# Performance work log

Hardware: AMD Instinct MI355X
Metric: run time of the kernel (lower is better)

## Reference

```python
import jax, jax.numpy as jnp
import numpy as np

L, NH, H, V, MAXP = 12, 12, 768, 50257, 1024
HD = H // NH
EPS = 1e-5


def setup_inputs() -> dict:
    key = jax.random.key(0)
    ks = iter(jax.random.split(key, 32))
    s = 0.02
    inp = {
        "input_ids": jax.random.randint(next(ks), (8, 1024), 0, V),
        "tok_emb": jax.random.normal(next(ks), (V, H), jnp.float32) * s,
        "pos_emb": jax.random.normal(next(ks), (MAXP, H), jnp.float32) * s,
        "ln1_g": jnp.ones((L, H), jnp.float32),
        "ln1_b": jnp.zeros((L, H), jnp.float32),
        "w_attn": jax.random.normal(next(ks), (L, H, 3 * H), jnp.float32) * s,
        "b_attn": jnp.zeros((L, 3 * H), jnp.float32),
        "w_out": jax.random.normal(next(ks), (L, H, H), jnp.float32) * s,
        "b_out": jnp.zeros((L, H), jnp.float32),
        "ln2_g": jnp.ones((L, H), jnp.float32),
        "ln2_b": jnp.zeros((L, H), jnp.float32),
        "w1": jax.random.normal(next(ks), (L, H, 4 * H), jnp.float32) * s,
        "b1": jnp.zeros((L, 4 * H), jnp.float32),
        "w2": jax.random.normal(next(ks), (L, 4 * H, H), jnp.float32) * s,
        "b2": jnp.zeros((L, H), jnp.float32),
        "lnf_g": jnp.ones((H,), jnp.float32),
        "lnf_b": jnp.zeros((H,), jnp.float32),
    }
    return inp


def _ln(x, g, b):
    mu = jnp.mean(x, axis=-1, keepdims=True)
    var = jnp.var(x, axis=-1, keepdims=True)
    return (x - mu) * jax.lax.rsqrt(var + EPS) * g + b


def _gpt2_forward(input_ids, tok_emb, pos_emb, ln1_g, ln1_b, w_attn, b_attn,
                  w_out, b_out, ln2_g, ln2_b, w1, b1, w2, b2, lnf_g, lnf_b):
    B, S = input_ids.shape
    x = tok_emb[input_ids] + pos_emb[:S]  # [B,S,H]
    # causal mask: True above the diagonal (future positions)
    mask = jnp.triu(jnp.ones((S, S), dtype=bool), k=1)
    inv_sqrt_hd = 1.0 / np.sqrt(HD)
    for l in range(L):
        n1 = _ln(x, ln1_g[l], ln1_b[l])
        qkv = n1 @ w_attn[l] + b_attn[l]  # [B,S,3H]
        q, k, v = jnp.split(qkv, 3, axis=-1)
        q = q.reshape(B, S, NH, HD).transpose(0, 2, 1, 3)
        k = k.reshape(B, S, NH, HD).transpose(0, 2, 1, 3)
        v = v.reshape(B, S, NH, HD).transpose(0, 2, 1, 3)
        scores = jnp.einsum('bhtd,bhsd->bhts', q, k)  # [B,NH,S,S]
        # faithful to source: mask with -10000 BEFORE dividing by sqrt(head_size)
        scores = jnp.where(mask, -10000.0, scores) * inv_sqrt_hd
        probs = jax.nn.softmax(scores, axis=-1)
        attn = jnp.einsum('bhts,bhsd->bhtd', probs, v)
        attn = attn.transpose(0, 2, 1, 3).reshape(B, S, H)
        attn = attn @ w_out[l] + b_out[l]
        x = x + attn
        n2 = _ln(x, ln2_g[l], ln2_b[l])
        h = jax.nn.gelu(n2 @ w1[l] + b1[l], approximate=False)
        x = x + (h @ w2[l] + b2[l])
    x = _ln(x, lnf_g, lnf_b)
    final_encoding = x[:, -1]  # [B,H]
    logits = final_encoding @ tok_emb.T  # tied weights, [B,V]
    return logits, final_encoding


def reference(input_ids, tok_emb, pos_emb, ln1_g, ln1_b, w_attn, b_attn,
              w_out, b_out, ln2_g, ln2_b, w1, b1, w2, b2, lnf_g, lnf_b):
    return _gpt2_forward(input_ids, tok_emb, pos_emb, ln1_g, ln1_b, w_attn,
                         b_attn, w_out, b_out, ln2_g, ln2_b, w1, b1, w2, b2,
                         lnf_g, lnf_b)
```

## Files before the change

kernel.cpp:

```cpp
#include <hip/hip_runtime.h>
#include <cmath>

typedef unsigned short u16;
typedef __bf16 bf16;
typedef __attribute__((ext_vector_type(8))) bf16 bf16x8;
typedef __attribute__((ext_vector_type(4))) float f32x4;

#define DINL __device__ __forceinline__

#define BB 8
#define SS 1024
#define HH 768
#define LL 12
#define NHH 12
#define HDD 64
#define MM 8192
#define VV 50257

DINL u16 f2bf(float f) {
    unsigned int u = __builtin_bit_cast(unsigned int, f);
    u += 0x7fff + ((u >> 16) & 1);
    return (u16)(u >> 16);
}

DINL bf16x8 ld_bf8(const u16* p) { return *(const bf16x8*)p; }

typedef __attribute__((address_space(1))) unsigned int as1_u32;
typedef __attribute__((address_space(3))) unsigned int as3_u32;

DINL void gllds16(const void* g, void* l) {
    __builtin_amdgcn_global_load_lds((as1_u32*)g, (as3_u32*)l, 16, 0, 0);
}

__global__ __launch_bounds__(256) void k_embed(const int* __restrict__ ids,
                                               const float* __restrict__ tok,
                                               const float* __restrict__ pos,
                                               float* __restrict__ x) {
    int tk = blockIdx.x;
    int s = tk & (SS - 1);
    int id = ids[tk];
    const float* tr = tok + (size_t)id * HH;
    const float* pr = pos + (size_t)s * HH;
    float* xr = x + (size_t)tk * HH;
#pragma unroll
    for (int j = 0; j < 3; j++) {
        int d = threadIdx.x + j * 256;
        xr[d] = tr[d] + pr[d];
    }
}

__global__ __launch_bounds__(256) void k_tcvt(const float* __restrict__ src, u16* __restrict__ dst,
                                              int R, int C, size_t sstr, size_t dstr) {
    src += (size_t)blockIdx.z * sstr;
    dst += (size_t)blockIdx.z * dstr;
    __shared__ float t[32][33];
    int tx = threadIdx.x & 31, ty = threadIdx.x >> 5;
    int c0 = blockIdx.x * 32, r0 = blockIdx.y * 32;
#pragma unroll
    for (int p = 0; p < 4; p++)
        t[ty + p * 8][tx] = src[(size_t)(r0 + ty + p * 8) * C + c0 + tx];
    __syncthreads();
#pragma unroll
    for (int p = 0; p < 4; p++)
        dst[(size_t)(c0 + ty + p * 8) * R + r0 + tx] = f2bf(t[tx][ty + p * 8]);
}

template <bool F32OUT>
__global__ __launch_bounds__(256) void k_ln(const float* __restrict__ x, const float* __restrict__ g,
                                            const float* __restrict__ b, void* __restrict__ outp,
                                            int nrows, int rs, int ro) {
    int w = threadIdx.x >> 6, lane = threadIdx.x & 63;
    int row = blockIdx.x * 4 + w;
    if (row >= nrows) return;
    const float4* xr = (const float4*)(x + ((size_t)row * rs + ro) * HH);
    float4 v[3];
    float s = 0.f, s2 = 0.f;
#pragma unroll
    for (int j = 0; j < 3; j++) {
        v[j] = xr[lane + 64 * j];
        s += v[j].x + v[j].y + v[j].z + v[j].w;
        s2 += v[j].x * v[j].x + v[j].y * v[j].y + v[j].z * v[j].z + v[j].w * v[j].w;
    }
#pragma unroll
    for (int off = 32; off; off >>= 1) {
        s += __shfl_xor(s, off, 64);
        s2 += __shfl_xor(s2, off, 64);
    }
    float mu = s * (1.0f / HH);
    float rstd = rsqrtf(s2 * (1.0f / HH) - mu * mu + 1e-5f);
#pragma unroll
    for (int j = 0; j < 3; j++) {
        int d4 = lane + 64 * j;
        float4 gv = ((const float4*)g)[d4];
        float4 bv = ((const float4*)b)[d4];
        float o0 = (v[j].x - mu) * rstd * gv.x + bv.x;
        float o1 = (v[j].y - mu) * rstd * gv.y + bv.y;
        float o2 = (v[j].z - mu) * rstd * gv.z + bv.z;
        float o3 = (v[j].w - mu) * rstd * gv.w + bv.w;
        if (F32OUT) {
            ((float4*)outp)[(size_t)row * (HH / 4) + d4] = make_float4(o0, o1, o2, o3);
        } else {
            ushort4 pk;
            pk.x = f2bf(o0); pk.y = f2bf(o1); pk.z = f2bf(o2); pk.w = f2bf(o3);
            *(ushort4*)((u16*)outp + (size_t)row * HH + d4 * 4) = pk;
        }
    }
}

template <int EPI>
__global__ __launch_bounds__(256) void k_gemm(const u16* __restrict__ A, const u16* __restrict__ BT,
                                              const float* __restrict__ bias, float* __restrict__ xio,
                                              u16* __restrict__ obuf, u16* __restrict__ qb,
                                              u16* __restrict__ kb, u16* __restrict__ vb,
                                              int N, int K) {
    __shared__ u16 As[2][128 * 32];
    __shared__ u16 Bs[2][128 * 32];
    const int t = threadIdx.x, w = t >> 6, lane = t & 63;
    const int l15 = lane & 15, l4 = lane >> 4;
    const int wr = w >> 1, wc = w & 1;
    const int m0 = blockIdx.y * 128, n0 = blockIdx.x * 128;
    const int KT = K >> 5;

    f32x4 acc[4][4] = {};

    auto stage = [&](int buf, int kt) {
#pragma unroll
        for (int i = 0; i < 2; i++) {
            int idx = w * 2 + i;
            int row = idx * 16 + (lane >> 2);
            int kc = kt * 32 + (((lane & 3) ^ ((lane >> 3) & 3)) * 8);
            gllds16(A + (size_t)(m0 + row) * K + kc, &As[buf][idx * 512]);
            gllds16(BT + (size_t)(n0 + row) * K + kc, &Bs[buf][idx * 512]);
        }
    };

    stage(0, 0);
    __syncthreads();
    int buf = 0;
    const int sw = (l15 >> 1) & 3;
    for (int kt = 0; kt < KT; ++kt) {
        if (kt + 1 < KT) stage(buf ^ 1, kt + 1);
        bf16x8 af[4], bfr[4];
#pragma unroll
        for (int i = 0; i < 4; i++) af[i] = ld_bf8(&As[buf][(wr * 64 + i * 16 + l15) * 32 + ((l4 ^ sw) * 8)]);
#pragma unroll
        for (int j = 0; j < 4; j++) bfr[j] = ld_bf8(&Bs[buf][(wc * 64 + j * 16 + l15) * 32 + ((l4 ^ sw) * 8)]);
#pragma unroll
        for (int i = 0; i < 4; i++)
#pragma unroll
            for (int j = 0; j < 4; j++)
                acc[i][j] = __builtin_amdgcn_mfma_f32_16x16x32_bf16(af[i], bfr[j], acc[i][j], 0, 0, 0);
        __syncthreads();
        buf ^= 1;
    }

#pragma unroll
    for (int i = 0; i < 4; i++) {
#pragma unroll
        for (int j = 0; j < 4; j++) {
#pragma unroll
            for (int r = 0; r < 4; r++) {
                int row = m0 + wr * 64 + i * 16 + l4 * 4 + r;
                int n = n0 + wc * 64 + j * 16 + l15;
                float v = acc[i][j][r] + bias[n];
                if (EPI == 0) {
                    int seg = n / HH, wi = n % HH;
                    int h = wi >> 6, d = wi & 63;
                    int bi = row >> 10, s = row & (SS - 1);
                    size_t bh = (size_t)(bi * NHH + h);
                    if (seg == 0)
                        qb[(bh * SS + s) * HDD + d] = f2bf(v);
                    else if (seg == 1)
                        kb[(bh * SS + s) * HDD + d] = f2bf(v);
                    else
                        vb[(bh * HDD + d) * SS + s] = f2bf(v);
                } else if (EPI == 1) {
                    xio[(size_t)row * N + n] += v;
                } else {
                    float gl = 0.5f * v * (1.0f + erff(v * 0.70710678118654752f));
                    obuf[(size_t)row * N + n] = f2bf(gl);
                }
            }
        }
    }
}

__global__ __launch_bounds__(256) void k_gemm64(const u16* __restrict__ A, const u16* __restrict__ BT,
                                                const float* __restrict__ bias, float* __restrict__ xio,
                                                int N, int K) {
    __shared__ u16 As[2][128 * 32];
    __shared__ u16 Bs[2][64 * 32];
    const int t = threadIdx.x, w = t >> 6, lane = t & 63;
    const int l15 = lane & 15, l4 = lane >> 4;
    const int wr = w >> 1, wc = w & 1;
    const int m0 = blockIdx.y * 128, n0 = blockIdx.x * 64;
    const int KT = K >> 5;

    f32x4 acc[4][2] = {};

    auto stage = [&](int buf, int kt) {
        int rr = lane >> 2;
        int kc = kt * 32 + (((lane & 3) ^ ((lane >> 3) & 3)) * 8);
#pragma unroll
        for (int i = 0; i < 2; i++) {
            int idx = w * 2 + i;
            gllds16(A + (size_t)(m0 + idx * 16 + rr) * K + kc, &As[buf][idx * 512]);
        }
        gllds16(BT + (size_t)(n0 + w * 16 + rr) * K + kc, &Bs[buf][w * 512]);
    };

    stage(0, 0);
    __syncthreads();
    int buf = 0;
    const int sw = (l15 >> 1) & 3;
    for (int kt = 0; kt < KT; ++kt) {
        if (kt + 1 < KT) stage(buf ^ 1, kt + 1);
        bf16x8 af[4], bfr[2];
#pragma unroll
        for (int i = 0; i < 4; i++) af[i] = ld_bf8(&As[buf][(wr * 64 + i * 16 + l15) * 32 + ((l4 ^ sw) * 8)]);
#pragma unroll
        for (int j = 0; j < 2; j++) bfr[j] = ld_bf8(&Bs[buf][(wc * 32 + j * 16 + l15) * 32 + ((l4 ^ sw) * 8)]);
#pragma unroll
        for (int i = 0; i < 4; i++)
#pragma unroll
            for (int j = 0; j < 2; j++)
                acc[i][j] = __builtin_amdgcn_mfma_f32_16x16x32_bf16(af[i], bfr[j], acc[i][j], 0, 0, 0);
        __syncthreads();
        buf ^= 1;
    }

#pragma unroll
    for (int i = 0; i < 4; i++) {
#pragma unroll
        for (int j = 0; j < 2; j++) {
#pragma unroll
            for (int r = 0; r < 4; r++) {
                int row = m0 + wr * 64 + i * 16 + l4 * 4 + r;
                int n = n0 + wc * 32 + j * 16 + l15;
                xio[(size_t)row * N + n] += acc[i][j][r] + bias[n];
            }
        }
    }
}

__global__ __launch_bounds__(256) void k_attn(const u16* __restrict__ q, const u16* __restrict__ k,
                                              const u16* __restrict__ vt, u16* __restrict__ o) {
    int qt = 15 - blockIdx.x;
    int bh = blockIdx.y;
    int w = threadIdx.x >> 6, lane = threadIdx.x & 63;
    int l15 = lane & 15, l4 = lane >> 4;

    __shared__ u16 Ks[2][64 * 64];
    __shared__ u16 Vs[2][64 * 64];
    __shared__ u16 pl[4][16 * 72];
    u16* pw = pl[w];

    const size_t bhq = (size_t)bh * SS * HDD;
    int qrow0 = qt * 64 + w * 16;

    auto stage = [&](int buf, int kvb) {
#pragma unroll
        for (int i = 0; i < 2; i++) {
            int rl = w * 16 + i * 8 + (lane >> 3);
            int c = lane & 7;
            int sc = (c ^ (rl & 7)) * 8;
            gllds16(k + bhq + (size_t)(kvb * 64 + rl) * HDD + sc, &Ks[buf][(w * 16 + i * 8) * 64]);
            gllds16(vt + ((size_t)bh * HDD + rl) * SS + kvb * 64 + sc, &Vs[buf][(w * 16 + i * 8) * 64]);
        }
    };

    bf16x8 aq[2];
#pragma unroll
    for (int ks = 0; ks < 2; ks++)
        aq[ks] = ld_bf8(q + bhq + (size_t)(qrow0 + l15) * HDD + ks * 32 + l4 * 8);

    f32x4 acc[4] = {};
    float mrun[4], lrun[4];
#pragma unroll
    for (int r = 0; r < 4; r++) { mrun[r] = -1e30f; lrun[r] = 0.f; }

    stage(0, 0);
    __syncthreads();
    int buf = 0;

    for (int kvb = 0; kvb <= qt; ++kvb) {
        if (kvb < qt) stage(buf ^ 1, kvb + 1);

        f32x4 s[4] = {};
#pragma unroll
        for (int c = 0; c < 4; c++) {
#pragma unroll
            for (int ks = 0; ks < 2; ks++) {
                bf16x8 kf = ld_bf8(&Ks[buf][(c * 16 + l15) * 64 + ((ks * 4 + l4) ^ (l15 & 7)) * 8]);
                s[c] = __builtin_amdgcn_mfma_f32_16x16x32_bf16(aq[ks], kf, s[c], 0, 0, 0);
            }
        }
        bool diag = (kvb == qt);
        float rmax[4] = {-1e30f, -1e30f, -1e30f, -1e30f};
#pragma unroll
        for (int c = 0; c < 4; c++) {
#pragma unroll
            for (int r = 0; r < 4; r++) {
                float val = s[c][r] * 0.125f;
                if (diag) {
                    int kvi = kvb * 64 + c * 16 + l15;
                    int qi = qrow0 + l4 * 4 + r;
                    if (kvi > qi) val = -1250.0f;
                }
                s[c][r] = val;
                rmax[r] = fmaxf(rmax[r], val);
            }
        }
#pragma unroll
        for (int off = 1; off < 16; off <<= 1)
#pragma unroll
            for (int r = 0; r < 4; r++) rmax[r] = fmaxf(rmax[r], __shfl_xor(rmax[r], off, 64));
        float ef[4];
#pragma unroll
        for (int r = 0; r < 4; r++) {
            float mnew = fmaxf(mrun[r], rmax[r]);
            ef[r] = __expf(mrun[r] - mnew);
            mrun[r] = mnew;
        }
        float rsum[4] = {0.f, 0.f, 0.f, 0.f};
#pragma unroll
        for (int c = 0; c < 4; c++)
#pragma unroll
            for (int r = 0; r < 4; r++) {
                float pv = __expf(s[c][r] - mrun[r]);
                s[c][r] = pv;
                rsum[r] += pv;
            }
#pragma unroll
        for (int off = 1; off < 16; off <<= 1)
#pragma unroll
            for (int r = 0; r < 4; r++) rsum[r] += __shfl_xor(rsum[r], off, 64);
#pragma unroll
        for (int r = 0; r < 4; r++) lrun[r] = lrun[r] * ef[r] + rsum[r];
#pragma unroll
        for (int cd = 0; cd < 4; cd++)
#pragma unroll
            for (int r = 0; r < 4; r++) acc[cd][r] *= ef[r];
#pragma unroll
        for (int c = 0; c < 4; c++)
#pragma unroll
            for (int r = 0; r < 4; r++)
                pw[(l4 * 4 + r) * 72 + c * 16 + l15] = f2bf(s[c][r]);
#pragma unroll
        for (int ks = 0; ks < 2; ks++) {
            bf16x8 pa = ld_bf8(pw + l15 * 72 + ks * 32 + l4 * 8);
#pragma unroll
            for (int cd = 0; cd < 4; cd++) {
                bf16x8 vf = ld_bf8(&Vs[buf][(cd * 16 + l15) * 64 + ((ks * 4 + l4) ^ (l15 & 7)) * 8]);
                acc[cd] = __builtin_amdgcn_mfma_f32_16x16x32_bf16(pa, vf, acc[cd], 0, 0, 0);
            }
        }
        __syncthreads();
        buf ^= 1;
    }

    int b = bh / NHH, h = bh % NHH;
#pragma unroll
    for (int cd = 0; cd < 4; cd++) {
#pragma unroll
        for (int r = 0; r < 4; r++) {
            int qi = qrow0 + l4 * 4 + r;
            float ov = acc[cd][r] / lrun[r];
            o[((size_t)b * SS + qi) * HH + h * HDD + cd * 16 + l15] = f2bf(ov);
        }
    }
}

__global__ __launch_bounds__(256) void k_logits(const float* __restrict__ enc,
                                                const float* __restrict__ tok,
                                                float* __restrict__ out) {
    int w = threadIdx.x >> 6, lane = threadIdx.x & 63;
    int v = blockIdx.x * 4 + w;
    if (v >= VV) return;
    const float4* tr = (const float4*)(tok + (size_t)v * HH);
    float a[8];
#pragma unroll
    for (int b = 0; b < 8; b++) a[b] = 0.f;
#pragma unroll
    for (int j = 0; j < 3; j++) {
        float4 t4 = tr[lane + 64 * j];
#pragma unroll
        for (int b = 0; b < 8; b++) {
            float4 e4 = *(const float4*)(enc + (size_t)b * HH + (lane + 64 * j) * 4);
            a[b] += t4.x * e4.x + t4.y * e4.y + t4.z * e4.z + t4.w * e4.w;
        }
    }
#pragma unroll
    for (int off = 32; off; off >>= 1)
#pragma unroll
        for (int b = 0; b < 8; b++) a[b] += __shfl_xor(a[b], off, 64);
    if (lane == 0) {
#pragma unroll
        for (int b = 0; b < 8; b++) out[(size_t)b * VV + v] = a[b];
    }
}

extern "C" void kernel_launch(void* const* d_in, const int* in_sizes, int n_in,
                              void* d_out, int out_size, void* d_ws, size_t ws_size,
                              hipStream_t stream) {
    const int* ids = (const int*)d_in[0];
    const float* tok = (const float*)d_in[1];
    const float* pos = (const float*)d_in[2];
    const float* ln1g = (const float*)d_in[3];
    const float* ln1b = (const float*)d_in[4];
    const float* wat = (const float*)d_in[5];
    const float* bat = (const float*)d_in[6];
    const float* wou = (const float*)d_in[7];
    const float* bou = (const float*)d_in[8];
    const float* ln2g = (const float*)d_in[9];
    const float* ln2b = (const float*)d_in[10];
    const float* w1 = (const float*)d_in[11];
    const float* b1 = (const float*)d_in[12];
    const float* w2 = (const float*)d_in[13];
    const float* b2 = (const float*)d_in[14];
    const float* lnfg = (const float*)d_in[15];
    const float* lnfb = (const float*)d_in[16];

    char* ws = (char*)d_ws;
    float* xw = (float*)(ws + 0);
    u16* nb = (u16*)(ws + 25165824);
    u16* qb = (u16*)(ws + 37748736);
    u16* kb = (u16*)(ws + 50331648);
    u16* vb = (u16*)(ws + 62914560);
    u16* ab = (u16*)(ws + 75497472);
    u16* hb = (u16*)(ws + 88080384);
    u16* wt = (u16*)(ws + 138412032);
    const size_t LSTR = 7077888;
    const size_t WAO = 0, WOO = 1769472, W1O = 2359296, W2O = 4718592;

    float* outf = (float*)d_out;
    float* enc = outf + (size_t)BB * VV;

    k_embed<<<MM, 256, 0, stream>>>(ids, tok, pos, xw);
    k_tcvt<<<dim3(72, 24, 12), 256, 0, stream>>>(wat, wt + WAO, 768, 2304, (size_t)768 * 2304, LSTR);
    k_tcvt<<<dim3(24, 24, 12), 256, 0, stream>>>(wou, wt + WOO, 768, 768, (size_t)768 * 768, LSTR);
    k_tcvt<<<dim3(96, 24, 12), 256, 0, stream>>>(w1, wt + W1O, 768, 3072, (size_t)768 * 3072, LSTR);
    k_tcvt<<<dim3(24, 96, 12), 256, 0, stream>>>(w2, wt + W2O, 3072, 768, (size_t)3072 * 768, LSTR);

    for (int l = 0; l < LL; l++) {
        const u16* wl = wt + (size_t)l * LSTR;
        k_ln<false><<<MM / 4, 256, 0, stream>>>(xw, ln1g + l * HH, ln1b + l * HH, nb, MM, 1, 0);
        k_gemm<0><<<dim3(18, 64), 256, 0, stream>>>(nb, wl + WAO, bat + (size_t)l * 2304,
                                                    nullptr, nullptr, qb, kb, vb, 2304, 768);
        k_attn<<<dim3(16, 96), 256, 0, stream>>>(qb, kb, vb, ab);
        k_gemm64<<<dim3(12, 64), 256, 0, stream>>>(ab, wl + WOO, bou + (size_t)l * HH, xw, 768, 768);
        k_ln<false><<<MM / 4, 256, 0, stream>>>(xw, ln2g + l * HH, ln2b + l * HH, nb, MM, 1, 0);
        k_gemm<2><<<dim3(24, 64), 256, 0, stream>>>(nb, wl + W1O, b1 + (size_t)l * 3072,
                                                    nullptr, hb, nullptr, nullptr, nullptr, 3072, 768);
        k_gemm64<<<dim3(12, 64), 256, 0, stream>>>(hb, wl + W2O, b2 + (size_t)l * HH, xw, 768, 3072);
    }
    k_ln<true><<<2, 256, 0, stream>>>(xw, lnfg, lnfb, enc, BB, SS, SS - 1);
    k_logits<<<(VV + 3) / 4, 256, 0, stream>>>(enc, tok, outf);
}
```

Measured before the change: 4.369 ms.

## Remap GEMM tiles across XCDs and use lazy rescaling in flash attention

Remaps GEMM block indices so that consecutive M tiles land on the same XCD, with the aim of improving L2 reuse of the shared B tiles. In the attention kernel, the per-block row max and sum shuffles are replaced by a lazy-rescale scheme. The running max is updated, and the accumulators rescaled, only when some lane's local max exceeds the running max by more than 8. Per-lane partial sums are kept and reduced once at the end. This removes most cross-lane shuffles and exp rescales per KV block, but allows exponentials up to e^8 in bf16 probabilities, which slightly changes numerics.

```diff
diff --git a/kernel.cpp b/kernel.cpp
--- a/kernel.cpp
+++ b/kernel.cpp
@@ -30,6 +30,13 @@
 
 DINL void gllds16(const void* g, void* l) {
     __builtin_amdgcn_global_load_lds((as1_u32*)g, (as3_u32*)l, 16, 0, 0);
+}
+
+DINL void xcd_remap(int gx, int& mTile, int& nTile) {
+    int i = blockIdx.y * gx + blockIdx.x;
+    int xcd = i & 7, j = i >> 3;
+    nTile = j % gx;
+    mTile = (j / gx) * 8 + xcd;
 }
 
 __global__ __launch_bounds__(256) void k_embed(const int* __restrict__ ids,
@@ -118,7 +125,9 @@
     const int t = threadIdx.x, w = t >> 6, lane = t & 63;
     const int l15 = lane & 15, l4 = lane >> 4;
     const int wr = w >> 1, wc = w & 1;
-    const int m0 = blockIdx.y * 128, n0 = blockIdx.x * 128;
+    int mT, nT;
+    xcd_remap(gridDim.x, mT, nT);
+    const int m0 = mT * 128, n0 = nT * 128;
     const int KT = K >> 5;
 
     f32x4 acc[4][4] = {};
@@ -193,7 +202,9 @@
     const int t = threadIdx.x, w = t >> 6, lane = t & 63;
     const int l15 = lane & 15, l4 = lane >> 4;
     const int wr = w >> 1, wc = w & 1;
-    const int m0 = blockIdx.y * 128, n0 = blockIdx.x * 64;
+    int mT, nT;
+    xcd_remap(gridDim.x, mT, nT);
+    const int m0 = mT * 128, n0 = nT * 64;
     const int KT = K >> 5;
 
     f32x4 acc[4][2] = {};
@@ -275,9 +286,9 @@
         aq[ks] = ld_bf8(q + bhq + (size_t)(qrow0 + l15) * HDD + ks * 32 + l4 * 8);
 
     f32x4 acc[4] = {};
-    float mrun[4], lrun[4];
-#pragma unroll
-    for (int r = 0; r < 4; r++) { mrun[r] = -1e30f; lrun[r] = 0.f; }
+    float mrun[4], psum[4];
+#pragma unroll
+    for (int r = 0; r < 4; r++) { mrun[r] = -1e30f; psum[r] = 0.f; }
 
     stage(0, 0);
     __syncthreads();
@@ -296,7 +307,6 @@
             }
         }
         bool diag = (kvb == qt);
-        float rmax[4] = {-1e30f, -1e30f, -1e30f, -1e30f};
 #pragma unroll
         for (int c = 0; c < 4; c++) {
 #pragma unroll
@@ -308,44 +318,38 @@
                     if (kvi > qi) val = -1250.0f;
                 }
                 s[c][r] = val;
-                rmax[r] = fmaxf(rmax[r], val);
-            }
-        }
-#pragma unroll
-        for (int off = 1; off < 16; off <<= 1)
-#pragma unroll
-            for (int r = 0; r < 4; r++) rmax[r] = fmaxf(rmax[r], __shfl_xor(rmax[r], off, 64));
-        float ef[4];
-#pragma unroll
-        for (int r = 0; r < 4; r++) {
-            float mnew = fmaxf(mrun[r], rmax[r]);
-            ef[r] = __expf(mrun[r] - mnew);
-            mrun[r] = mnew;
-        }
-        float rsum[4] = {0.f, 0.f, 0.f, 0.f};
+            }
+        }
+        float lmax[4];
+#pragma unroll
+        for (int r = 0; r < 4; r++)
+            lmax[r] = fmaxf(fmaxf(s[0][r], s[1][r]), fmaxf(s[2][r], s[3][r]));
+        int ok = 1;
+#pragma unroll
+        for (int r = 0; r < 4; r++) ok &= (lmax[r] <= mrun[r] + 8.f) ? 1 : 0;
+        if (!__all(ok)) {
+#pragma unroll
+            for (int off = 1; off < 16; off <<= 1)
+#pragma unroll
+                for (int r = 0; r < 4; r++) lmax[r] = fmaxf(lmax[r], __shfl_xor(lmax[r], off, 64));
+#pragma unroll
+            for (int r = 0; r < 4; r++) {
+                float mnew = fmaxf(mrun[r], lmax[r]);
+                float ef = __expf(mrun[r] - mnew);
+                mrun[r] = mnew;
+                psum[r] *= ef;
+#pragma unroll
+                for (int cd = 0; cd < 4; cd++) acc[cd][r] *= ef;
+            }
+        }
 #pragma unroll
         for (int c = 0; c < 4; c++)
 #pragma unroll
             for (int r = 0; r < 4; r++) {
                 float pv = __expf(s[c][r] - mrun[r]);
-                s[c][r] = pv;
-                rsum[r] += pv;
-            }
-#pragma unroll
-        for (int off = 1; off < 16; off <<= 1)
-#pragma unroll
-            for (int r = 0; r < 4; r++) rsum[r] += __shfl_xor(rsum[r], off, 64);
-#pragma unroll
-        for (int r = 0; r < 4; r++) lrun[r] = lrun[r] * ef[r] + rsum[r];
-#pragma unroll
-        for (int cd = 0; cd < 4; cd++)
-#pragma unroll
-            for (int r = 0; r < 4; r++) acc[cd][r] *= ef[r];
-#pragma unroll
-        for (int c = 0; c < 4; c++)
-#pragma unroll
-            for (int r = 0; r < 4; r++)
-                pw[(l4 * 4 + r) * 72 + c * 16 + l15] = f2bf(s[c][r]);
+                psum[r] += pv;
+                pw[(l4 * 4 + r) * 72 + c * 16 + l15] = f2bf(pv);
+            }
 #pragma unroll
         for (int ks = 0; ks < 2; ks++) {
             bf16x8 pa = ld_bf8(pw + l15 * 72 + ks * 32 + l4 * 8);
@@ -359,13 +363,18 @@
         buf ^= 1;
     }
 
+#pragma unroll
+    for (int off = 1; off < 16; off <<= 1)
+#pragma unroll
+        for (int r = 0; r < 4; r++) psum[r] += __shfl_xor(psum[r], off, 64);
+
     int b = bh / NHH, h = bh % NHH;
 #pragma unroll
     for (int cd = 0; cd < 4; cd++) {
 #pragma unroll
         for (int r = 0; r < 4; r++) {
             int qi = qrow0 + l4 * 4 + r;
-            float ov = acc[cd][r] / lrun[r];
+            float ov = acc[cd][r] / psum[r];
             o[((size_t)b * SS + qi) * HH + h * HDD + cd * 16 + l15] = f2bf(ov);
         }
     }
```

Result: faster. 3.899 ms (-10.7%).
